# Performance work log

Hardware: AMD Instinct MI355X
Metric: run time of the kernel (lower is better)

Reference implementation:

```python
import jax, jax.numpy as jnp
import numpy as np

D = 256       # d_model
B = 64        # batch
N_JOBS = 16
N_OPS = 8
S = N_JOBS * N_OPS  # seq_len = 128


def setup_inputs() -> dict:
    key = jax.random.key(0)
    ks = jax.random.split(key, 10)
    enc = jax.random.normal(ks[0], (B, S, D), jnp.float32)
    # S_seq: (job_id, op_id) grid -> each job has N_OPS ops in order
    job = jnp.arange(S, dtype=jnp.int32) // N_OPS
    op = jnp.arange(S, dtype=jnp.int32) % N_OPS
    S_seq = jnp.broadcast_to(jnp.stack([job, op], -1)[None], (B, S, 2)).astype(jnp.int32)
    s = 1.0 / np.sqrt(D)
    u = lambda k, shape: jax.random.uniform(k, shape, jnp.float32, -s, s)
    return {
        "encoder_outputs": enc,
        "S_seq": S_seq,
        "W_ih": u(ks[1], (4 * D, D)),   # LSTM input weights (i,f,g,o)
        "W_hh": u(ks[2], (4 * D, D)),
        "b_ih": u(ks[3], (4 * D,)),
        "b_hh": u(ks[4], (4 * D,)),
        "W1": u(ks[5], (D, 2 * D)),     # pointer_attention Linear(2D, D)
        "b1": u(ks[6], (D,)),
        "W2": u(ks[7], (1, D)),         # pointer_attention Linear(D, 1)
        "b2": u(ks[8], (1,)),
    }


def reference(encoder_outputs, S_seq, W_ih, W_hh, b_ih, b_hh, W1, b1, W2, b2):
    B_, S_, D_ = encoder_outputs.shape
    jobs = S_seq[:, :, 0]
    ops = S_seq[:, :, 1]
    batch_idx = jnp.arange(B_)
    # split pointer MLP first layer into query / encoder parts (same math as
    # concat([q, enc]) @ W1.T); encoder part is step-invariant -> precompute.
    Wq, We = W1[:, :D_], W1[:, D_:]
    enc_proj = jnp.einsum('bsd,hd->bsh', encoder_outputs, We) + b1  # [B,S,D]

    dec_h0 = encoder_outputs.mean(axis=1)          # [B,D] initial decoder input
    h0 = jnp.zeros((B_, D_), encoder_outputs.dtype)
    c0 = jnp.zeros((B_, D_), encoder_outputs.dtype)
    M_sched0 = jnp.zeros((B_, S_), bool)
    M_mask0 = ops > 0                              # precedence: only op 0 of each job free

    def step(carry, _):
        h, c, dec_h, M_sched, M_mask = carry
        # --- LSTM cell (PyTorch gate order i,f,g,o) ---
        gates = dec_h @ W_ih.T + b_ih + h @ W_hh.T + b_hh
        i, f, g, o = jnp.split(gates, 4, axis=-1)
        c_new = jax.nn.sigmoid(f) * c + jax.nn.sigmoid(i) * jnp.tanh(g)
        h_new = jax.nn.sigmoid(o) * jnp.tanh(c_new)
        # --- pointer attention scores ---
        act = jnp.tanh(enc_proj + (h_new @ Wq.T)[:, None, :])      # [B,S,D]
        scores = jnp.einsum('bsd,d->bs', act, W2[0]) + b2[0]       # [B,S]
        masked = jnp.where(M_sched | M_mask, -jnp.inf, scores)
        logp = jax.nn.log_softmax(masked, axis=-1)
        chosen = jnp.argmax(masked, axis=-1)                       # greedy (training=False)
        lp = logp[batch_idx, chosen]
        # --- mask updates ---
        M_sched = M_sched.at[batch_idx, chosen].set(True)
        cj = jobs[batch_idx, chosen]
        co = ops[batch_idx, chosen]
        unlock = (jobs == cj[:, None]) & (ops == (co + 1)[:, None])
        M_mask = jnp.where(unlock, False, M_mask)
        dec_h_new = encoder_outputs[batch_idx, chosen]             # [B,D]
        return (h_new, c_new, dec_h_new, M_sched, M_mask), (chosen, lp)

    carry0 = (h0, c0, dec_h0, M_sched0, M_mask0)
    _, (chosen_seq, logp_seq) = jax.lax.scan(step, carry0, None, length=S_)
    return chosen_seq.T, logp_seq.T  # [B,S] each
```

## Files before the change

### kernel.cpp

```cpp
#include <hip/hip_runtime.h>

#define NBATCH 64
#define NS     128
#define ND     256

static __device__ __forceinline__ float fexp2(float x){ return __builtin_amdgcn_exp2f(x); }
static __device__ __forceinline__ float frcp (float x){ return __builtin_amdgcn_rcpf(x); }
static __device__ __forceinline__ float fast_exp(float x){ return fexp2(x*1.4426950408889634f); }
static __device__ __forceinline__ float fast_log(float x){ return __builtin_amdgcn_logf(x)*0.6931471805599453f; }
static __device__ __forceinline__ float fast_tanh(float x){
  float e = fexp2(x*2.8853900817779268f);
  return 1.0f - 2.0f*frcp(e+1.0f);
}
static __device__ __forceinline__ float fast_sig(float x){
  return frcp(1.0f + fexp2(-1.4426950408889634f*x));
}

static __device__ __forceinline__ void st_cc(float* p, float v){
  __hip_atomic_store(p, v, __ATOMIC_RELAXED, __HIP_MEMORY_SCOPE_AGENT);
}
static __device__ __forceinline__ float ld_cc(const float* p){
  return __hip_atomic_load(p, __ATOMIC_RELAXED, __HIP_MEMORY_SCOPE_AGENT);
}
static __device__ __forceinline__ void st_ci(int* p, int v){
  __hip_atomic_store(p, v, __ATOMIC_RELAXED, __HIP_MEMORY_SCOPE_AGENT);
}
static __device__ __forceinline__ int ld_ci(const int* p){
  return __hip_atomic_load(p, __ATOMIC_RELAXED, __HIP_MEMORY_SCOPE_AGENT);
}
static __device__ __forceinline__ void drain(){ asm volatile("s_waitcnt vmcnt(0)" ::: "memory"); }

__global__ void k_transpose_w1(const float* __restrict__ W1, float* __restrict__ Wt){
  __shared__ float tile[64*65];
  int di = blockIdx.x >> 2;
  int hi = blockIdx.x & 3;
  int tid = threadIdx.x;
  #pragma unroll
  for (int r=0;r<16;++r){
    int lin = tid + r*256;
    int h = lin >> 6, d = lin & 63;
    tile[h*65 + d] = W1[(hi*64+h)*512 + di*64 + d];
  }
  __syncthreads();
  #pragma unroll
  for (int r=0;r<16;++r){
    int lin = tid + r*256;
    int d = lin >> 6, h = lin & 63;
    Wt[(di*64+d)*256 + hi*64 + h] = tile[h*65 + d];
  }
}

__global__ void k_dec0(const float* __restrict__ enc, float* __restrict__ dec0){
  int b = blockIdx.x, d = threadIdx.x;
  float s = 0.f;
  for (int t=0;t<NS;++t) s += enc[(b*NS+t)*ND + d];
  dec0[b*ND+d] = s * (1.0f/(float)NS);
}

__global__ void k_encproj(const float* __restrict__ enc, const float* __restrict__ Wt,
                          const float* __restrict__ b1, float* __restrict__ ep2){
  __shared__ float enc_l[8*256];
  int b = blockIdx.x >> 4, sg = blockIdx.x & 15;
  int tid = threadIdx.x;
  #pragma unroll
  for (int r=0;r<8;++r){
    int lin = tid + r*256;
    enc_l[lin] = enc[(b*NS + sg*8)*ND + lin];
  }
  __syncthreads();
  float acc[8];
  float bb = b1[tid];
  #pragma unroll
  for (int k=0;k<8;++k) acc[k] = bb;
  for (int d=0; d<ND; ++d){
    float w = Wt[(ND + d)*ND + tid];
    #pragma unroll
    for (int k=0;k<8;++k) acc[k] = fmaf(enc_l[k*256+d], w, acc[k]);
  }
  int qtr = tid >> 6, hh = tid & 63;
  #pragma unroll
  for (int k=0;k<8;++k)
    ep2[((b*4 + qtr)*NS + (sg*8+k))*64 + hh] = acc[k];
}

__global__ void __launch_bounds__(256)
k_decode(const float* __restrict__ enc,
         const float* __restrict__ W_ih, const float* __restrict__ W_hh,
         const float* __restrict__ b_ih, const float* __restrict__ b_hh,
         const float* __restrict__ Wt,   const float* __restrict__ W2,
         const float* __restrict__ b2p,
         const float* __restrict__ ep2,  const float* __restrict__ dec0,
         float* __restrict__ hbuf, float* __restrict__ qbuf,
         float* __restrict__ P,   float* __restrict__ out,
         int* __restrict__ qflag, int* __restrict__ pflag)
{
  __shared__ float4 x_swz[8*16*8];
  __shared__ __align__(16) float ep_l[128*66];
  __shared__ __align__(16) float q4_l[4*64];
  __shared__ __align__(16) float q_l[64];
  __shared__ __align__(16) float w2_l[64];
  __shared__ float hn_l[8*8];
  __shared__ float sc_l[128];
  __shared__ int   chosen_l[8];
  __shared__ unsigned int msched[8][4];
  __shared__ unsigned int mmask[8][4];

  const int tid  = threadIdx.x;
  const int bid  = blockIdx.x;
  const int o    = bid & 31;
  const int beta = bid >> 5;
  const int b2   = bid >> 2;
  const int qtr  = bid & 3;

  const int u  = tid >> 3;
  const int ks = tid & 7;
  const int dd = u >> 2;
  const int g  = u & 3;
  const int dglob = o*8 + dd;

  float4 wreg[16];
  {
    const float* src = (ks < 4) ? (W_ih + (g*ND + dglob)*ND + ks*64)
                                : (W_hh + (g*ND + dglob)*ND + (ks-4)*64);
    const float4* s4 = (const float4*)src;
    #pragma unroll
    for (int i=0;i<16;++i) wreg[i] = s4[i];
  }
  const float bias_r = b_ih[g*ND + dglob] + b_hh[g*ND + dglob];
  float wq[8];
  #pragma unroll
  for (int d8=0; d8<8; ++d8) wq[d8] = Wt[(o*8+d8)*ND + tid];

  for (int i = tid; i < 128*64; i += 256){
    int s = i >> 6, hh = i & 63;
    ep_l[s*66 + hh] = ep2[((b2*4 + qtr)*NS + s)*64 + hh];
  }
  if (tid < 64) w2_l[tid] = W2[qtr*64 + tid];
  if (tid < 8){
    #pragma unroll
    for (int w=0;w<4;++w){ msched[tid][w] = 0u; mmask[tid][w] = 0xFEFEFEFEu; }
  }
  float creg[8];
  #pragma unroll
  for (int i=0;i<8;++i) creg[i]=0.f;

  const float b2v = b2p[0];
  const float NINF = -__builtin_inff();

  const int blc = tid >> 5;
  const int l32 = tid & 31;
  const int bglob = beta*8 + blc;
  const int kbase = l32*16;

  for (int t = 0; t <= NS; ++t){
    if (t > 0){
      if (tid < 32){
        while (true){
          int v = ld_ci(&pflag[beta*32 + tid]);
          if (__all(v >= t)) break;
        }
      }
      __syncthreads();

      float pq[16];
      #pragma unroll
      for (int j=0;j<16;++j){
        int k = j>>2, q = j&3, s = l32+32*k;
        pq[j] = ld_cc(&P[(bglob*4+q)*NS + s]);
      }
      float vals[4];
      float bv = NINF; int bi = 0x7fffffff;
      #pragma unroll
      for (int k=0;k<4;++k){
        int s = l32 + 32*k;
        float sc = pq[k*4+0]+pq[k*4+1]+pq[k*4+2]+pq[k*4+3] + b2v;
        unsigned int mb = ((msched[blc][s>>5] | mmask[blc][s>>5]) >> (s&31)) & 1u;
        float mv = mb ? NINF : sc;
        vals[k] = mv;
        if (mv > bv || (mv == bv && s < bi)){ bv = mv; bi = s; }
      }
      #pragma unroll
      for (int m=1; m<32; m<<=1){
        float ov = __shfl_xor(bv, m);
        int   oi = __shfl_xor(bi, m);
        if (ov > bv || (ov == bv && oi < bi)){ bv = ov; bi = oi; }
      }
      float ssum = 0.f;
      #pragma unroll
      for (int k=0;k<4;++k) ssum += fast_exp(vals[k] - bv);
      #pragma unroll
      for (int m=1; m<32; m<<=1) ssum += __shfl_xor(ssum, m);
      if (l32 == 0){
        msched[blc][bi>>5] |= (1u << (bi & 31));
        if ((bi & 7) != 7){ int nb = bi+1; mmask[blc][nb>>5] &= ~(1u << (nb & 31)); }
        chosen_l[blc] = bi;
        if (o == 0){
          out[bglob*NS + (t-1)] = (float)bi;
          out[NBATCH*NS + bglob*NS + (t-1)] = -fast_log(ssum);
        }
      }
    }
    if (t == NS) break;

    if (kbase < 256){
      const float* dsrc = (t == 0) ? (dec0 + bglob*ND)
                                   : (enc + (bglob*NS + chosen_l[blc])*ND);
      const float4* s4 = (const float4*)dsrc + (kbase>>2);
      #pragma unroll
      for (int j=0;j<4;++j){
        int k = kbase + j*4;
        x_swz[(blc*16 + ((k & 63) >> 2))*8 + (k >> 6)] = s4[j];
      }
    } else if (t == 0){
      #pragma unroll
      for (int j=0;j<4;++j){
        int k = kbase + j*4;
        x_swz[(blc*16 + ((k & 63) >> 2))*8 + (k >> 6)] = make_float4(0.f,0.f,0.f,0.f);
      }
    }
    __syncthreads();

    const float4* xb = x_swz + ks;
    #pragma unroll
    for (int bl=0; bl<8; ++bl){
      float acc = 0.f;
      #pragma unroll
      for (int i=0;i<16;++i){
        float4 xv = xb[(bl*16 + i)*8];
        acc = fmaf(xv.x, wreg[i].x, acc);
        acc = fmaf(xv.y, wreg[i].y, acc);
        acc = fmaf(xv.z, wreg[i].z, acc);
        acc = fmaf(xv.w, wreg[i].w, acc);
      }
      acc += __shfl_xor(acc, 1);
      acc += __shfl_xor(acc, 2);
      acc += __shfl_xor(acc, 4);
      acc += bias_r;
      float vf = __shfl_xor(acc, 8);
      float vg = __shfl_xor(acc, 16);
      float vo = __shfl_xor(acc, 24);
      if (g == 0){
        float cn = fast_sig(vf)*creg[bl] + fast_sig(acc)*fast_tanh(vg);
        creg[bl] = cn;
        float hn = fast_sig(vo)*fast_tanh(cn);
        if (ks == 0) hn_l[bl*8 + dd] = hn;
      }
    }
    __syncthreads();

    #pragma unroll
    for (int bl=0; bl<8; ++bl){
      float a = 0.f;
      #pragma unroll
      for (int d8=0; d8<8; ++d8) a = fmaf(hn_l[bl*8+d8], wq[d8], a);
      st_cc(&qbuf[((beta*8+bl)*32 + o)*ND + tid], a);
    }
    if (tid < 64){
      int bl = tid >> 3, d8 = tid & 7;
      st_cc(&hbuf[((t+1)&1)*NBATCH*ND + (beta*8+bl)*ND + o*8 + d8], hn_l[bl*8+d8]);
    }
    drain();
    __syncthreads();
    if (tid == 0) st_ci(&qflag[beta*32 + o], t+1);

    if (tid < 32){
      while (true){
        int v = ld_ci(&qflag[beta*32 + tid]);
        if (__all(v >= t+1)) break;
      }
    }
    __syncthreads();
    {
      int oq = tid >> 6, h = tid & 63;
      float a = 0.f;
      #pragma unroll
      for (int i=0;i<8;++i) a += ld_cc(&qbuf[(b2*32 + oq*8 + i)*ND + qtr*64 + h]);
      q4_l[oq*64 + h] = a;
    }
    __syncthreads();
    if (tid < 64) q_l[tid] = q4_l[tid] + q4_l[64+tid] + q4_l[128+tid] + q4_l[192+tid];
    __syncthreads();
    {
      int s = tid >> 1, half = tid & 1;
      const float2* epv = (const float2*)(ep_l + s*66 + half*32);
      const float2* qv  = (const float2*)(q_l  + half*32);
      const float2* wv  = (const float2*)(w2_l + half*32);
      float a = 0.f;
      #pragma unroll
      for (int j=0;j<16;++j){
        float2 e = epv[j], qq = qv[j], ww = wv[j];
        a = fmaf(fast_tanh(e.x + qq.x), ww.x, a);
        a = fmaf(fast_tanh(e.y + qq.y), ww.y, a);
      }
      a += __shfl_xor(a, 1);
      if (half == 0) sc_l[s] = a;
    }
    __syncthreads();
    if (tid < 128) st_cc(&P[(b2*4 + qtr)*NS + tid], sc_l[tid]);
    drain();
    __syncthreads();
    if (tid == 0) st_ci(&pflag[b2*4 + qtr], t+1);

    if (t+1 < NS && kbase >= 256){
      const float* hp = hbuf + ((t+1)&1)*NBATCH*ND + bglob*ND + (kbase-256);
      float v[16];
      #pragma unroll
      for (int j=0;j<16;++j) v[j] = ld_cc(hp+j);
      float* xs = (float*)x_swz;
      #pragma unroll
      for (int j=0;j<16;++j){
        int k = kbase + j;
        xs[((blc*16 + ((k&63)>>2))*8 + (k>>6))*4 + (k&3)] = v[j];
      }
    }
  }
}

extern "C" void kernel_launch(void* const* d_in, const int* in_sizes, int n_in,
                              void* d_out, int out_size, void* d_ws, size_t ws_size,
                              hipStream_t stream){
  const float* enc  = (const float*)d_in[0];
  const float* W_ih = (const float*)d_in[2];
  const float* W_hh = (const float*)d_in[3];
  const float* b_ih = (const float*)d_in[4];
  const float* b_hh = (const float*)d_in[5];
  const float* W1   = (const float*)d_in[6];
  const float* b1   = (const float*)d_in[7];
  const float* W2   = (const float*)d_in[8];
  const float* b2   = (const float*)d_in[9];
  float* out = (float*)d_out;

  int*   qflag = (int*)d_ws;
  int*   pflag = qflag + 256;
  float* qbuf  = (float*)(pflag + 256);
  float* P     = qbuf + (size_t)NBATCH*32*ND;
  float* hbuf  = P    + (size_t)NBATCH*4*NS;
  float* ep2   = hbuf + (size_t)2*NBATCH*ND;
  float* Wt    = ep2  + (size_t)64*4*128*64;
  float* dec0  = Wt   + 512*256;

  hipMemsetAsync(d_ws, 0, 512*sizeof(int), stream);
  hipLaunchKernelGGL(k_transpose_w1, dim3(32),   dim3(256), 0, stream, W1, Wt);
  hipLaunchKernelGGL(k_dec0,         dim3(64),   dim3(256), 0, stream, enc, dec0);
  hipLaunchKernelGGL(k_encproj,      dim3(1024), dim3(256), 0, stream, enc, Wt, b1, ep2);

  void* args[] = { (void*)&enc, (void*)&W_ih, (void*)&W_hh, (void*)&b_ih, (void*)&b_hh,
                   (void*)&Wt, (void*)&W2, (void*)&b2, (void*)&ep2, (void*)&dec0,
                   (void*)&hbuf, (void*)&qbuf, (void*)&P, (void*)&out,
                   (void*)&qflag, (void*)&pflag };
  hipLaunchCooperativeKernel((void*)k_decode, dim3(256), dim3(256), args, 0, stream);
}
```

Baseline: 1.501 ms.

## Compute pointer scores per batch in 64 blocks and publish chosen index via flag word

The pointer-attention phase moves from all 256 blocks (each handling a quarter of d for 4 batches, with partial scores exchanged through global P and a second grid flag) to 64 designated blocks. Each of these computes the full 256-wide score for one batch row, reading enc_proj straight from global memory, then runs argmax/log-softmax locally and publishes the choice together with the step number in a single cword. This removes one global partial-score exchange and one cross-block barrier per step. In exchange, 192 blocks sit idle during scoring, the active blocks do four times the tanh work, and ep2 is read from L2 every step instead of from LDS. The h-state prefetch is also kept in registers, and a non-cooperative fallback launch is added.

```diff
diff --git a/kernel.cpp b/kernel.cpp
--- a/kernel.cpp
+++ b/kernel.cpp
@@ -77,10 +77,9 @@
     #pragma unroll
     for (int k=0;k<8;++k) acc[k] = fmaf(enc_l[k*256+d], w, acc[k]);
   }
-  int qtr = tid >> 6, hh = tid & 63;
   #pragma unroll
   for (int k=0;k<8;++k)
-    ep2[((b*4 + qtr)*NS + (sg*8+k))*64 + hh] = acc[k];
+    ep2[(b*NS + sg*8 + k)*ND + tid] = acc[k];
 }
 
 __global__ void __launch_bounds__(256)
@@ -91,26 +90,24 @@
          const float* __restrict__ b2p,
          const float* __restrict__ ep2,  const float* __restrict__ dec0,
          float* __restrict__ hbuf, float* __restrict__ qbuf,
-         float* __restrict__ P,   float* __restrict__ out,
-         int* __restrict__ qflag, int* __restrict__ pflag)
+         float* __restrict__ out,
+         int* __restrict__ flagv, int* __restrict__ cword)
 {
   __shared__ float4 x_swz[8*16*8];
-  __shared__ __align__(16) float ep_l[128*66];
-  __shared__ __align__(16) float q4_l[4*64];
-  __shared__ __align__(16) float q_l[64];
-  __shared__ __align__(16) float w2_l[64];
-  __shared__ float hn_l[8*8];
+  __shared__ __align__(16) float q_l[256];
+  __shared__ __align__(16) float w2_l[256];
   __shared__ float sc_l[128];
-  __shared__ int   chosen_l[8];
-  __shared__ unsigned int msched[8][4];
-  __shared__ unsigned int mmask[8][4];
+  __shared__ float hn_l[64];
+  __shared__ int   cw_l[8];
+  __shared__ unsigned int msched_l[4];
+  __shared__ unsigned int mmask_l[4];
 
   const int tid  = threadIdx.x;
   const int bid  = blockIdx.x;
   const int o    = bid & 31;
   const int beta = bid >> 5;
-  const int b2   = bid >> 2;
-  const int qtr  = bid & 3;
+  const bool is_batch = (o < 8);
+  const int my_b = beta*8 + o;
 
   const int u  = tid >> 3;
   const int ks = tid & 7;
@@ -131,80 +128,34 @@
   #pragma unroll
   for (int d8=0; d8<8; ++d8) wq[d8] = Wt[(o*8+d8)*ND + tid];
 
-  for (int i = tid; i < 128*64; i += 256){
-    int s = i >> 6, hh = i & 63;
-    ep_l[s*66 + hh] = ep2[((b2*4 + qtr)*NS + s)*64 + hh];
-  }
-  if (tid < 64) w2_l[tid] = W2[qtr*64 + tid];
-  if (tid < 8){
-    #pragma unroll
-    for (int w=0;w<4;++w){ msched[tid][w] = 0u; mmask[tid][w] = 0xFEFEFEFEu; }
-  }
+  if (is_batch) w2_l[tid] = W2[tid];
+  if (tid < 4){ msched_l[tid] = 0u; mmask_l[tid] = 0xFEFEFEFEu; }
+
   float creg[8];
   #pragma unroll
   for (int i=0;i<8;++i) creg[i]=0.f;
+  float hreg[16];
 
   const float b2v = b2p[0];
   const float NINF = -__builtin_inff();
-
   const int blc = tid >> 5;
   const int l32 = tid & 31;
   const int bglob = beta*8 + blc;
   const int kbase = l32*16;
 
-  for (int t = 0; t <= NS; ++t){
+  for (int t = 0; t < NS; ++t){
     if (t > 0){
-      if (tid < 32){
-        while (true){
-          int v = ld_ci(&pflag[beta*32 + tid]);
-          if (__all(v >= t)) break;
-        }
-      }
-      __syncthreads();
-
-      float pq[16];
-      #pragma unroll
-      for (int j=0;j<16;++j){
-        int k = j>>2, q = j&3, s = l32+32*k;
-        pq[j] = ld_cc(&P[(bglob*4+q)*NS + s]);
-      }
-      float vals[4];
-      float bv = NINF; int bi = 0x7fffffff;
-      #pragma unroll
-      for (int k=0;k<4;++k){
-        int s = l32 + 32*k;
-        float sc = pq[k*4+0]+pq[k*4+1]+pq[k*4+2]+pq[k*4+3] + b2v;
-        unsigned int mb = ((msched[blc][s>>5] | mmask[blc][s>>5]) >> (s&31)) & 1u;
-        float mv = mb ? NINF : sc;
-        vals[k] = mv;
-        if (mv > bv || (mv == bv && s < bi)){ bv = mv; bi = s; }
-      }
-      #pragma unroll
-      for (int m=1; m<32; m<<=1){
-        float ov = __shfl_xor(bv, m);
-        int   oi = __shfl_xor(bi, m);
-        if (ov > bv || (ov == bv && oi < bi)){ bv = ov; bi = oi; }
-      }
-      float ssum = 0.f;
-      #pragma unroll
-      for (int k=0;k<4;++k) ssum += fast_exp(vals[k] - bv);
-      #pragma unroll
-      for (int m=1; m<32; m<<=1) ssum += __shfl_xor(ssum, m);
-      if (l32 == 0){
-        msched[blc][bi>>5] |= (1u << (bi & 31));
-        if ((bi & 7) != 7){ int nb = bi+1; mmask[blc][nb>>5] &= ~(1u << (nb & 31)); }
-        chosen_l[blc] = bi;
-        if (o == 0){
-          out[bglob*NS + (t-1)] = (float)bi;
-          out[NBATCH*NS + bglob*NS + (t-1)] = -fast_log(ssum);
-        }
-      }
-    }
-    if (t == NS) break;
+      if (tid < 8){
+        int v;
+        do { v = ld_ci(&cword[beta*8 + tid]); } while (!__all((v >> 8) >= t));
+        cw_l[tid] = v & 255;
+      }
+    }
+    __syncthreads();
 
     if (kbase < 256){
       const float* dsrc = (t == 0) ? (dec0 + bglob*ND)
-                                   : (enc + (bglob*NS + chosen_l[blc])*ND);
+                                   : (enc + (bglob*NS + cw_l[blc])*ND);
       const float4* s4 = (const float4*)dsrc + (kbase>>2);
       #pragma unroll
       for (int j=0;j<4;++j){
@@ -216,6 +167,13 @@
       for (int j=0;j<4;++j){
         int k = kbase + j*4;
         x_swz[(blc*16 + ((k & 63) >> 2))*8 + (k >> 6)] = make_float4(0.f,0.f,0.f,0.f);
+      }
+    } else {
+      float* xs = (float*)x_swz;
+      #pragma unroll
+      for (int j=0;j<16;++j){
+        int k = kbase + j;
+        xs[((blc*16 + ((k&63)>>2))*8 + (k>>6))*4 + (k&3)] = hreg[j];
       }
     }
     __syncthreads();
@@ -261,57 +219,76 @@
     }
     drain();
     __syncthreads();
-    if (tid == 0) st_ci(&qflag[beta*32 + o], t+1);
+    if (tid == 0) st_ci(&flagv[beta*32 + o], t+1);
 
     if (tid < 32){
-      while (true){
-        int v = ld_ci(&qflag[beta*32 + tid]);
-        if (__all(v >= t+1)) break;
-      }
-    }
-    __syncthreads();
-    {
-      int oq = tid >> 6, h = tid & 63;
+      int v;
+      do { v = ld_ci(&flagv[beta*32 + tid]); } while (!__all(v >= t+1));
+    }
+    __syncthreads();
+
+    if (is_batch){
+      float qv = 0.f;
+      #pragma unroll
+      for (int o2=0; o2<32; ++o2) qv += ld_cc(&qbuf[(my_b*32 + o2)*ND + tid]);
+      q_l[tid] = qv;
+    }
+    __syncthreads();
+
+    if (is_batch){
+      int s = tid >> 1, half = tid & 1;
+      const float4* epv = (const float4*)(ep2 + ((size_t)my_b*NS + s)*ND + half*128);
+      const float4* qv4 = (const float4*)(q_l  + half*128);
+      const float4* wv  = (const float4*)(w2_l + half*128);
       float a = 0.f;
       #pragma unroll
-      for (int i=0;i<8;++i) a += ld_cc(&qbuf[(b2*32 + oq*8 + i)*ND + qtr*64 + h]);
-      q4_l[oq*64 + h] = a;
-    }
-    __syncthreads();
-    if (tid < 64) q_l[tid] = q4_l[tid] + q4_l[64+tid] + q4_l[128+tid] + q4_l[192+tid];
-    __syncthreads();
-    {
-      int s = tid >> 1, half = tid & 1;
-      const float2* epv = (const float2*)(ep_l + s*66 + half*32);
-      const float2* qv  = (const float2*)(q_l  + half*32);
-      const float2* wv  = (const float2*)(w2_l + half*32);
-      float a = 0.f;
-      #pragma unroll
-      for (int j=0;j<16;++j){
-        float2 e = epv[j], qq = qv[j], ww = wv[j];
+      for (int j=0;j<32;++j){
+        float4 e = epv[j], qq = qv4[j], ww = wv[j];
         a = fmaf(fast_tanh(e.x + qq.x), ww.x, a);
         a = fmaf(fast_tanh(e.y + qq.y), ww.y, a);
+        a = fmaf(fast_tanh(e.z + qq.z), ww.z, a);
+        a = fmaf(fast_tanh(e.w + qq.w), ww.w, a);
       }
       a += __shfl_xor(a, 1);
-      if (half == 0) sc_l[s] = a;
-    }
-    __syncthreads();
-    if (tid < 128) st_cc(&P[(b2*4 + qtr)*NS + tid], sc_l[tid]);
-    drain();
-    __syncthreads();
-    if (tid == 0) st_ci(&pflag[b2*4 + qtr], t+1);
+      if (half == 0) sc_l[s] = a + b2v;
+    }
+    __syncthreads();
+
+    if (is_batch && tid < 32){
+      float vals[4];
+      float bv = NINF; int bi = 0x7fffffff;
+      #pragma unroll
+      for (int k=0;k<4;++k){
+        int s = tid + 32*k;
+        unsigned int mb = ((msched_l[k] | mmask_l[k]) >> (s & 31)) & 1u;
+        float mv = mb ? NINF : sc_l[s];
+        vals[k] = mv;
+        if (mv > bv || (mv == bv && s < bi)){ bv = mv; bi = s; }
+      }
+      #pragma unroll
+      for (int m=1; m<32; m<<=1){
+        float ov = __shfl_xor(bv, m);
+        int   oi = __shfl_xor(bi, m);
+        if (ov > bv || (ov == bv && oi < bi)){ bv = ov; bi = oi; }
+      }
+      float ssum = 0.f;
+      #pragma unroll
+      for (int k=0;k<4;++k) ssum += fast_exp(vals[k] - bv);
+      #pragma unroll
+      for (int m=1; m<32; m<<=1) ssum += __shfl_xor(ssum, m);
+      if (tid == 0){
+        msched_l[bi>>5] |= (1u << (bi & 31));
+        if ((bi & 7) != 7){ int nb = bi+1; mmask_l[nb>>5] &= ~(1u << (nb & 31)); }
+        out[my_b*NS + t] = (float)bi;
+        out[NBATCH*NS + my_b*NS + t] = -fast_log(ssum);
+        st_ci(&cword[my_b], ((t+1) << 8) | bi);
+      }
+    }
 
     if (t+1 < NS && kbase >= 256){
       const float* hp = hbuf + ((t+1)&1)*NBATCH*ND + bglob*ND + (kbase-256);
-      float v[16];
-      #pragma unroll
-      for (int j=0;j<16;++j) v[j] = ld_cc(hp+j);
-      float* xs = (float*)x_swz;
-      #pragma unroll
-      for (int j=0;j<16;++j){
-        int k = kbase + j;
-        xs[((blc*16 + ((k&63)>>2))*8 + (k>>6))*4 + (k&3)] = v[j];
-      }
+      #pragma unroll
+      for (int j=0;j<16;++j) hreg[j] = ld_cc(hp+j);
     }
   }
 }
@@ -330,23 +307,29 @@
   const float* b2   = (const float*)d_in[9];
   float* out = (float*)d_out;
 
-  int*   qflag = (int*)d_ws;
-  int*   pflag = qflag + 256;
-  float* qbuf  = (float*)(pflag + 256);
-  float* P     = qbuf + (size_t)NBATCH*32*ND;
-  float* hbuf  = P    + (size_t)NBATCH*4*NS;
+  int*   flagv = (int*)d_ws;
+  int*   cword = flagv + 256;
+  float* qbuf  = (float*)(cword + 64);
+  float* hbuf  = qbuf + (size_t)NBATCH*32*ND;
   float* ep2   = hbuf + (size_t)2*NBATCH*ND;
-  float* Wt    = ep2  + (size_t)64*4*128*64;
+  float* Wt    = ep2  + (size_t)NBATCH*NS*ND;
   float* dec0  = Wt   + 512*256;
 
-  hipMemsetAsync(d_ws, 0, 512*sizeof(int), stream);
+  hipMemsetAsync(d_ws, 0, 320*sizeof(int), stream);
   hipLaunchKernelGGL(k_transpose_w1, dim3(32),   dim3(256), 0, stream, W1, Wt);
   hipLaunchKernelGGL(k_dec0,         dim3(64),   dim3(256), 0, stream, enc, dec0);
   hipLaunchKernelGGL(k_encproj,      dim3(1024), dim3(256), 0, stream, enc, Wt, b1, ep2);
 
   void* args[] = { (void*)&enc, (void*)&W_ih, (void*)&W_hh, (void*)&b_ih, (void*)&b_hh,
                    (void*)&Wt, (void*)&W2, (void*)&b2, (void*)&ep2, (void*)&dec0,
-                   (void*)&hbuf, (void*)&qbuf, (void*)&P, (void*)&out,
-                   (void*)&qflag, (void*)&pflag };
-  hipLaunchCooperativeKernel((void*)k_decode, dim3(256), dim3(256), args, 0, stream);
-}
+                   (void*)&hbuf, (void*)&qbuf, (void*)&out,
+                   (void*)&flagv, (void*)&cword };
+  hipError_t err = hipLaunchCooperativeKernel((void*)k_decode, dim3(256), dim3(256),
+                                              args, 0, stream);
+  if (err != hipSuccess){
+    (void)hipGetLastError();
+    hipLaunchKernelGGL(k_decode, dim3(256), dim3(256), 0, stream,
+                       enc, W_ih, W_hh, b_ih, b_hh, Wt, W2, b2, ep2, dec0,
+                       hbuf, qbuf, out, flagv, cword);
+  }
+}
```

Result: slower. 2.261 ms (+50.6%).

## Replace flag-based inter-block sync with tagged 64-bit value words

Applied to the files above, without the earlier changes.

Each value exchanged between blocks (q partials, h state, pointer scores) is now stored as a 64-bit word that packs the float with the step index as a tag. Consumers spin on the data words themselves until every tag matches, so the separate flag stores, vmcnt drains and the block barriers around the flag polling go away. This removes a round trip through global memory per exchange, but doubles the traffic for those buffers and makes every thread poll. The workspace memset grows to clear all tagged words, and a non-cooperative launch fallback is added.

```diff
diff --git a/kernel.cpp b/kernel.cpp
--- a/kernel.cpp
+++ b/kernel.cpp
@@ -3,6 +3,8 @@
 #define NBATCH 64
 #define NS     128
 #define ND     256
+
+typedef unsigned long long u64;
 
 static __device__ __forceinline__ float fexp2(float x){ return __builtin_amdgcn_exp2f(x); }
 static __device__ __forceinline__ float frcp (float x){ return __builtin_amdgcn_rcpf(x); }
@@ -16,19 +18,18 @@
   return frcp(1.0f + fexp2(-1.4426950408889634f*x));
 }
 
-static __device__ __forceinline__ void st_cc(float* p, float v){
+static __device__ __forceinline__ void st64(u64* p, u64 v){
   __hip_atomic_store(p, v, __ATOMIC_RELAXED, __HIP_MEMORY_SCOPE_AGENT);
 }
-static __device__ __forceinline__ float ld_cc(const float* p){
+static __device__ __forceinline__ u64 ld64(const u64* p){
   return __hip_atomic_load(p, __ATOMIC_RELAXED, __HIP_MEMORY_SCOPE_AGENT);
 }
-static __device__ __forceinline__ void st_ci(int* p, int v){
-  __hip_atomic_store(p, v, __ATOMIC_RELAXED, __HIP_MEMORY_SCOPE_AGENT);
-}
-static __device__ __forceinline__ int ld_ci(const int* p){
-  return __hip_atomic_load(p, __ATOMIC_RELAXED, __HIP_MEMORY_SCOPE_AGENT);
-}
-static __device__ __forceinline__ void drain(){ asm volatile("s_waitcnt vmcnt(0)" ::: "memory"); }
+static __device__ __forceinline__ u64 pk(float v, unsigned tag){
+  return ((u64)tag << 32) | (u64)__float_as_uint(v);
+}
+static __device__ __forceinline__ float upk(u64 w){
+  return __uint_as_float((unsigned)w);
+}
 
 __global__ void k_transpose_w1(const float* __restrict__ W1, float* __restrict__ Wt){
   __shared__ float tile[64*65];
@@ -90,9 +91,8 @@
          const float* __restrict__ Wt,   const float* __restrict__ W2,
          const float* __restrict__ b2p,
          const float* __restrict__ ep2,  const float* __restrict__ dec0,
-         float* __restrict__ hbuf, float* __restrict__ qbuf,
-         float* __restrict__ P,   float* __restrict__ out,
-         int* __restrict__ qflag, int* __restrict__ pflag)
+         u64* __restrict__ hT, u64* __restrict__ qT, u64* __restrict__ PT,
+         float* __restrict__ out)
 {
   __shared__ float4 x_swz[8*16*8];
   __shared__ __align__(16) float ep_l[128*66];
@@ -143,6 +143,7 @@
   float creg[8];
   #pragma unroll
   for (int i=0;i<8;++i) creg[i]=0.f;
+  float hreg[16];
 
   const float b2v = b2p[0];
   const float NINF = -__builtin_inff();
@@ -154,26 +155,28 @@
 
   for (int t = 0; t <= NS; ++t){
     if (t > 0){
-      if (tid < 32){
-        while (true){
-          int v = ld_ci(&pflag[beta*32 + tid]);
-          if (__all(v >= t)) break;
+      const unsigned tg = (unsigned)t;
+      u64 w[16]; unsigned st = 0xffffu;
+      do {
+        #pragma unroll
+        for (int j=0;j<16;++j){
+          if (st & (1u<<j)){
+            int k = j>>2, q = j&3, s = l32 + 32*k;
+            w[j] = ld64(&PT[(bglob*4+q)*NS + s]);
+          }
         }
-      }
-      __syncthreads();
-
-      float pq[16];
-      #pragma unroll
-      for (int j=0;j<16;++j){
-        int k = j>>2, q = j&3, s = l32+32*k;
-        pq[j] = ld_cc(&P[(bglob*4+q)*NS + s]);
-      }
+        unsigned ns = st;
+        #pragma unroll
+        for (int j=0;j<16;++j) if ((unsigned)(w[j]>>32) == tg) ns &= ~(1u<<j);
+        st = ns;
+      } while (st);
+
       float vals[4];
       float bv = NINF; int bi = 0x7fffffff;
       #pragma unroll
       for (int k=0;k<4;++k){
         int s = l32 + 32*k;
-        float sc = pq[k*4+0]+pq[k*4+1]+pq[k*4+2]+pq[k*4+3] + b2v;
+        float sc = upk(w[k*4+0]) + upk(w[k*4+1]) + upk(w[k*4+2]) + upk(w[k*4+3]) + b2v;
         unsigned int mb = ((msched[blc][s>>5] | mmask[blc][s>>5]) >> (s&31)) & 1u;
         float mv = mb ? NINF : sc;
         vals[k] = mv;
@@ -201,6 +204,7 @@
       }
     }
     if (t == NS) break;
+    __syncthreads();
 
     if (kbase < 256){
       const float* dsrc = (t == 0) ? (dec0 + bglob*ND)
@@ -216,6 +220,13 @@
       for (int j=0;j<4;++j){
         int k = kbase + j*4;
         x_swz[(blc*16 + ((k & 63) >> 2))*8 + (k >> 6)] = make_float4(0.f,0.f,0.f,0.f);
+      }
+    } else {
+      float* xs = (float*)x_swz;
+      #pragma unroll
+      for (int j=0;j<16;++j){
+        int k = kbase + j;
+        xs[((blc*16 + ((k&63)>>2))*8 + (k>>6))*4 + (k&3)] = hreg[j];
       }
     }
     __syncthreads();
@@ -253,28 +264,31 @@
       float a = 0.f;
       #pragma unroll
       for (int d8=0; d8<8; ++d8) a = fmaf(hn_l[bl*8+d8], wq[d8], a);
-      st_cc(&qbuf[((beta*8+bl)*32 + o)*ND + tid], a);
+      st64(&qT[((size_t)((beta*8+bl)*32 + o))*ND + tid], pk(a, (unsigned)(t+1)));
     }
     if (tid < 64){
       int bl = tid >> 3, d8 = tid & 7;
-      st_cc(&hbuf[((t+1)&1)*NBATCH*ND + (beta*8+bl)*ND + o*8 + d8], hn_l[bl*8+d8]);
-    }
-    drain();
-    __syncthreads();
-    if (tid == 0) st_ci(&qflag[beta*32 + o], t+1);
-
-    if (tid < 32){
-      while (true){
-        int v = ld_ci(&qflag[beta*32 + tid]);
-        if (__all(v >= t+1)) break;
-      }
-    }
-    __syncthreads();
+      st64(&hT[((t+1)&1)*NBATCH*ND + (beta*8+bl)*ND + o*8 + d8],
+           pk(hn_l[bl*8+d8], (unsigned)(t+1)));
+    }
+
     {
       int oq = tid >> 6, h = tid & 63;
+      const unsigned tg = (unsigned)(t+1);
+      u64 w[8]; unsigned st = 0xffu;
+      do {
+        #pragma unroll
+        for (int i=0;i<8;++i)
+          if (st & (1u<<i))
+            w[i] = ld64(&qT[((size_t)(b2*32 + oq*8 + i))*ND + qtr*64 + h]);
+        unsigned ns = st;
+        #pragma unroll
+        for (int i=0;i<8;++i) if ((unsigned)(w[i]>>32) == tg) ns &= ~(1u<<i);
+        st = ns;
+      } while (st);
       float a = 0.f;
       #pragma unroll
-      for (int i=0;i<8;++i) a += ld_cc(&qbuf[(b2*32 + oq*8 + i)*ND + qtr*64 + h]);
+      for (int i=0;i<8;++i) a += upk(w[i]);
       q4_l[oq*64 + h] = a;
     }
     __syncthreads();
@@ -296,22 +310,22 @@
       if (half == 0) sc_l[s] = a;
     }
     __syncthreads();
-    if (tid < 128) st_cc(&P[(b2*4 + qtr)*NS + tid], sc_l[tid]);
-    drain();
-    __syncthreads();
-    if (tid == 0) st_ci(&pflag[b2*4 + qtr], t+1);
+    if (tid < 128) st64(&PT[(b2*4 + qtr)*NS + tid], pk(sc_l[tid], (unsigned)(t+1)));
 
     if (t+1 < NS && kbase >= 256){
-      const float* hp = hbuf + ((t+1)&1)*NBATCH*ND + bglob*ND + (kbase-256);
-      float v[16];
-      #pragma unroll
-      for (int j=0;j<16;++j) v[j] = ld_cc(hp+j);
-      float* xs = (float*)x_swz;
-      #pragma unroll
-      for (int j=0;j<16;++j){
-        int k = kbase + j;
-        xs[((blc*16 + ((k&63)>>2))*8 + (k>>6))*4 + (k&3)] = v[j];
-      }
+      const unsigned tg = (unsigned)(t+1);
+      const u64* hp = hT + ((t+1)&1)*NBATCH*ND + bglob*ND + (kbase-256);
+      u64 w[16]; unsigned st = 0xffffu;
+      do {
+        #pragma unroll
+        for (int j=0;j<16;++j) if (st & (1u<<j)) w[j] = ld64(hp + j);
+        unsigned ns = st;
+        #pragma unroll
+        for (int j=0;j<16;++j) if ((unsigned)(w[j]>>32) == tg) ns &= ~(1u<<j);
+        st = ns;
+      } while (st);
+      #pragma unroll
+      for (int j=0;j<16;++j) hreg[j] = upk(w[j]);
     }
   }
 }
@@ -330,23 +344,29 @@
   const float* b2   = (const float*)d_in[9];
   float* out = (float*)d_out;
 
-  int*   qflag = (int*)d_ws;
-  int*   pflag = qflag + 256;
-  float* qbuf  = (float*)(pflag + 256);
-  float* P     = qbuf + (size_t)NBATCH*32*ND;
-  float* hbuf  = P    + (size_t)NBATCH*4*NS;
-  float* ep2   = hbuf + (size_t)2*NBATCH*ND;
-  float* Wt    = ep2  + (size_t)64*4*128*64;
-  float* dec0  = Wt   + 512*256;
-
-  hipMemsetAsync(d_ws, 0, 512*sizeof(int), stream);
+  u64* qT = (u64*)d_ws;
+  u64* hT = qT + (size_t)NBATCH*32*ND;
+  u64* PT = hT + (size_t)2*NBATCH*ND;
+  const size_t tag_words = (size_t)NBATCH*32*ND + (size_t)2*NBATCH*ND + (size_t)NBATCH*4*NS;
+
+  float* ep2  = (float*)(PT + (size_t)NBATCH*4*NS);
+  float* Wt   = ep2 + (size_t)64*4*128*64;
+  float* dec0 = Wt  + 512*256;
+
+  hipMemsetAsync(d_ws, 0, tag_words*sizeof(u64), stream);
   hipLaunchKernelGGL(k_transpose_w1, dim3(32),   dim3(256), 0, stream, W1, Wt);
   hipLaunchKernelGGL(k_dec0,         dim3(64),   dim3(256), 0, stream, enc, dec0);
   hipLaunchKernelGGL(k_encproj,      dim3(1024), dim3(256), 0, stream, enc, Wt, b1, ep2);
 
   void* args[] = { (void*)&enc, (void*)&W_ih, (void*)&W_hh, (void*)&b_ih, (void*)&b_hh,
                    (void*)&Wt, (void*)&W2, (void*)&b2, (void*)&ep2, (void*)&dec0,
-                   (void*)&hbuf, (void*)&qbuf, (void*)&P, (void*)&out,
-                   (void*)&qflag, (void*)&pflag };
-  hipLaunchCooperativeKernel((void*)k_decode, dim3(256), dim3(256), args, 0, stream);
-}
+                   (void*)&hT, (void*)&qT, (void*)&PT, (void*)&out };
+  hipError_t err = hipLaunchCooperativeKernel((void*)k_decode, dim3(256), dim3(256),
+                                              args, 0, stream);
+  if (err != hipSuccess){
+    (void)hipGetLastError();
+    hipLaunchKernelGGL(k_decode, dim3(256), dim3(256), 0, stream,
+                       enc, W_ih, W_hh, b_ih, b_hh, Wt, W2, b2, ep2, dec0,
+                       hT, qT, PT, out);
+  }
+}
```

Result: slower. 1.780 ms (+18.5%).
